# Kernel optimization log

Hardware: AMD Instinct MI355X
Metric: run time of the kernel (lower is better)

Reference implementation:

```python
import jax, jax.numpy as jnp
import numpy as np

B, S, H, E, K = 4, 2048, 1024, 8, 2

def setup_inputs() -> dict:
    key = jax.random.key(0)
    k0, k1, k2, k3 = jax.random.split(key, 4)
    x = jax.random.normal(k0, (B, S, H), dtype=jnp.float32)
    # xavier-uniform-like scales
    router_w = jax.random.normal(k1, (E, H), dtype=jnp.float32) * np.float32(1.0 / np.sqrt(H))
    xav1 = np.float32(np.sqrt(2.0 / (2 * H + H)))
    w1 = jax.random.normal(k2, (E, 2 * H, H), dtype=jnp.float32) * xav1
    w2 = jax.random.normal(k3, (E, H, 2 * H), dtype=jnp.float32) * xav1
    return {"x": x, "router_w": router_w, "w1": w1, "w2": w2}

def reference(x, router_w, w1, w2):
    bsz, seq, hidden = x.shape
    n_experts = w1.shape[0]
    tokens = x.reshape(-1, hidden)                      # [T, H]
    T = tokens.shape[0]
    logits = tokens @ router_w.T                        # [T, E]
    topv, topi = jax.lax.top_k(logits, K)               # [T, K]
    w = jax.nn.softmax(topv, axis=-1).astype(tokens.dtype)
    # Dense gate matrix: gate[t, e] = routing weight of expert e for token t
    # (zero for non-selected experts). Equivalent to the torch pad/dispatch/
    # scatter-add combine: padded slots have weight 0 and contribute nothing.
    gate = jnp.zeros((T, n_experts), tokens.dtype).at[jnp.arange(T)[:, None], topi].add(w)
    out = jnp.zeros_like(tokens)
    for e in range(n_experts):  # small fixed expert count
        h = jax.nn.gelu(tokens @ w1[e].T, approximate=False)  # [T, 2H] (torch F.gelu = erf)
        y = h @ w2[e].T                                       # [T, H]
        out = out + gate[:, e:e + 1] * y
    return out.reshape(bsz, seq, hidden)
```

## Files before the change

### kernel.cpp

```cpp
#include <hip/hip_runtime.h>
#include <stdint.h>
#include <math.h>

#define T_TOK 8192
#define H_DIM 1024
#define H2    2048
#define NE    8

typedef unsigned short u16;
typedef __attribute__((ext_vector_type(8))) short bf16x8;
typedef __attribute__((ext_vector_type(4))) float f32x4;

__device__ __forceinline__ u16 f32_to_bf16(float f) {
  union { float f; unsigned u; } c; c.f = f;
  unsigned u = c.u + 0x7fffu + ((c.u >> 16) & 1u);
  return (u16)(u >> 16);
}
__device__ __forceinline__ float bf2f(u16 v) {
  union { unsigned u; float f; } c; c.u = (unsigned)v << 16; return c.f;
}

__device__ __forceinline__ float fast_gelu(float v) {
  float u = v * v;
  float z2 = v * fmaf(u, 0.1029437f, 2.3022078f);
  float e = __builtin_amdgcn_exp2f(z2);
  float r = __builtin_amdgcn_rcpf(1.0f + e);
  return v - v * r;
}

__device__ __forceinline__ void g2l16(const void* g, void* l) {
  __builtin_amdgcn_global_load_lds(
      (const __attribute__((address_space(1))) unsigned*)g,
      (__attribute__((address_space(3))) unsigned*)l, 16, 0, 0);
}

__global__ __launch_bounds__(256) void prep_kernel(
    const float* __restrict__ x, const float* __restrict__ rw,
    const float* __restrict__ w1, const float* __restrict__ w2,
    u16* __restrict__ xb, u16* __restrict__ w1b, u16* __restrict__ w2b,
    int* __restrict__ tope, float2* __restrict__ gate2) {
  int blk = blockIdx.x;
  if (blk < T_TOK / 4) {
    int wave = threadIdx.x >> 6;
    int lane = threadIdx.x & 63;
    int t = blk * 4 + wave;
    const float4* x4 = (const float4*)(x + (size_t)t * H_DIM);
    const float4* rw4 = (const float4*)rw;
    u16* xbrow = xb + (size_t)t * H_DIM;

    double acc[NE];
#pragma unroll
    for (int e = 0; e < NE; e++) acc[e] = 0.0;
#pragma unroll
    for (int i = 0; i < 4; i++) {
      int c = lane + 64 * i;
      float4 xv = x4[c];
      ushort4 bv = make_ushort4(f32_to_bf16(xv.x), f32_to_bf16(xv.y),
                                f32_to_bf16(xv.z), f32_to_bf16(xv.w));
      *(ushort4*)(xbrow + c * 4) = bv;
#pragma unroll
      for (int e = 0; e < NE; e++) {
        float4 wv = rw4[e * 256 + c];
        acc[e] += (double)xv.x * wv.x + (double)xv.y * wv.y +
                  (double)xv.z * wv.z + (double)xv.w * wv.w;
      }
    }
#pragma unroll
    for (int off = 32; off >= 1; off >>= 1)
#pragma unroll
      for (int e = 0; e < NE; e++) acc[e] += __shfl_xor(acc[e], off, 64);

    if (lane == 0) {
      int e0 = 0; double v0 = acc[0];
#pragma unroll
      for (int e = 1; e < NE; e++) if (acc[e] > v0) { v0 = acc[e]; e0 = e; }
      int e1 = -1; double v1 = -1e300;
#pragma unroll
      for (int e = 0; e < NE; e++) if (e != e0 && acc[e] > v1) { v1 = acc[e]; e1 = e; }
      double ex = exp(v1 - v0);
      tope[t] = e0 | (e1 << 8);
      gate2[t] = make_float2((float)(1.0 / (1.0 + ex)), (float)(ex / (1.0 + ex)));
    }
  } else {
    int cb = blk - T_TOK / 4;
    const float* src; u16* dst;
    if (cb < 1536) { src = w1; dst = w1b; }
    else           { src = w2; dst = w2b; cb -= 1536; }
    const int n4 = NE * H2 * H_DIM / 4;
    const int stride = 1536 * 256;
    const float4* s4 = (const float4*)src;
    for (int i = cb * 256 + threadIdx.x; i < n4; i += stride) {
      float4 v = s4[i];
      *(ushort4*)(dst + (size_t)i * 4) = make_ushort4(
          f32_to_bf16(v.x), f32_to_bf16(v.y), f32_to_bf16(v.z), f32_to_bf16(v.w));
    }
  }
}

__global__ __launch_bounds__(256) void build_kernel(
    const int* __restrict__ tope, int* __restrict__ counts,
    int* __restrict__ tok_list, int2* __restrict__ pos2) {
  __shared__ int cts[4][NE];
  __shared__ int gbase[NE];
  int tid = threadIdx.x, lane = tid & 63, w = tid >> 6;
  int t = blockIdx.x * 256 + tid;
  int pk = tope[t];
  int e0 = pk & 0xff, e1 = (pk >> 8) & 0xff;
  unsigned long long lt = ((unsigned long long)1 << lane) - 1;

  int r0 = 0, r1 = 0;
#pragma unroll
  for (int e = 0; e < NE; e++) {
    unsigned long long b0 = __ballot(e0 == e);
    unsigned long long b1 = __ballot(e1 == e);
    int n0 = __popcll(b0), n1 = __popcll(b1);
    if (e0 == e) r0 = __popcll(b0 & lt);
    if (e1 == e) r1 = n0 + __popcll(b1 & lt);
    if (lane == 0) cts[w][e] = n0 + n1;
  }
  __syncthreads();
  if (tid < NE) {
    int bt = cts[0][tid] + cts[1][tid] + cts[2][tid] + cts[3][tid];
    gbase[tid] = atomicAdd(&counts[tid], bt);
  }
  __syncthreads();
  int off0 = gbase[e0] + r0;
  int off1 = gbase[e1] + r1;
#pragma unroll
  for (int wp = 0; wp < 4; wp++) {
    if (wp < w) { off0 += cts[wp][e0]; off1 += cts[wp][e1]; }
  }
  tok_list[e0 * T_TOK + off0] = t;
  tok_list[e1 * T_TOK + off1] = t;
  pos2[t] = make_int2(off0, off1);
}

__global__ void prefix_kernel(const int* __restrict__ counts, int* __restrict__ hbase) {
  if (threadIdx.x == 0 && blockIdx.x == 0) {
    int b = 0;
    for (int e = 0; e < NE; e++) { hbase[e] = b; b += counts[e]; }
  }
}

__global__ __launch_bounds__(256) void g1_kernel(
    const u16* __restrict__ xb, const u16* __restrict__ w1b,
    u16* __restrict__ h, const int* __restrict__ tok_list,
    const int* __restrict__ counts, const int* __restrict__ hbase) {
  const int NT = H2 / 128;
  int e = blockIdx.x / (64 * NT);
  int rem = blockIdx.x % (64 * NT);
  int mt = rem / NT, nt = rem % NT;
  int cnt = counts[e];
  int m0 = mt * 128;
  if (m0 >= cnt) return;
  int base = hbase[e];

  __shared__ u16 As[128 * 64];
  __shared__ u16 Bs[128 * 64];

  int tid = threadIdx.x;
  int lane = tid & 63, wave = tid >> 6;
  int wr = wave >> 1, wc = wave & 1;
  int quad = lane >> 4, l16 = lane & 15;
  int srow = tid >> 3;
  int cg = (tid & 7) ^ (srow & 7);

  const u16* w1e = w1b + (size_t)e * H2 * H_DIM;
  const u16* ap[4]; const u16* bp[4];
#pragma unroll
  for (int R = 0; R < 4; R++) {
    int r = m0 + R * 32 + srow; if (r > cnt - 1) r = cnt - 1;
    ap[R] = xb + (size_t)tok_list[e * T_TOK + r] * H_DIM + cg * 8;
    bp[R] = w1e + (size_t)(nt * 128 + R * 32 + srow) * H_DIM + cg * 8;
  }

  f32x4 acc[4][4];
#pragma unroll
  for (int i = 0; i < 4; i++)
#pragma unroll
    for (int j = 0; j < 4; j++)
#pragma unroll
      for (int r = 0; r < 4; r++) acc[i][j][r] = 0.f;

  int swz = l16 & 7;
  for (int k0 = 0; k0 < H_DIM; k0 += 64) {
#pragma unroll
    for (int R = 0; R < 4; R++) {
      g2l16(ap[R] + k0, As + R * 2048 + tid * 8);
      g2l16(bp[R] + k0, Bs + R * 2048 + tid * 8);
    }
    __syncthreads();
#pragma unroll
    for (int kk = 0; kk < 2; kk++) {
      bf16x8 af[4], bfr[4];
      int q = kk * 4 + quad;
#pragma unroll
      for (int mi = 0; mi < 4; mi++)
        af[mi] = *(const bf16x8*)(As + (wr * 64 + mi * 16 + l16) * 64 + ((q ^ swz) * 8));
#pragma unroll
      for (int ni = 0; ni < 4; ni++)
        bfr[ni] = *(const bf16x8*)(Bs + (wc * 64 + ni * 16 + l16) * 64 + ((q ^ swz) * 8));
#pragma unroll
      for (int mi = 0; mi < 4; mi++)
#pragma unroll
        for (int ni = 0; ni < 4; ni++)
          acc[mi][ni] = __builtin_amdgcn_mfma_f32_16x16x32_bf16(af[mi], bfr[ni], acc[mi][ni], 0, 0, 0);
    }
    __syncthreads();
  }

#pragma unroll
  for (int mi = 0; mi < 4; mi++) {
    int rbase = wr * 64 + mi * 16 + quad * 4;
#pragma unroll
    for (int r = 0; r < 4; r++) {
      int rr = m0 + rbase + r;
      if (rr < cnt) {
        size_t ho = (size_t)(base + rr) * H2 + nt * 128 + wc * 64 + l16;
#pragma unroll
        for (int ni = 0; ni < 4; ni++)
          h[ho + ni * 16] = f32_to_bf16(fast_gelu(acc[mi][ni][r]));
      }
    }
  }
}

__global__ __launch_bounds__(256) void g2_kernel(
    const u16* __restrict__ h, const u16* __restrict__ w2b,
    u16* __restrict__ y,
    const int* __restrict__ counts, const int* __restrict__ hbase) {
  const int NT = H_DIM / 128;
  int e = blockIdx.x / (64 * NT);
  int rem = blockIdx.x % (64 * NT);
  int mt = rem / NT, nt = rem % NT;
  int cnt = counts[e];
  int m0 = mt * 128;
  if (m0 >= cnt) return;
  int base = hbase[e];

  __shared__ u16 As[128 * 64];
  __shared__ u16 Bs[128 * 64];

  int tid = threadIdx.x;
  int lane = tid & 63, wave = tid >> 6;
  int wr = wave >> 1, wc = wave & 1;
  int quad = lane >> 4, l16 = lane & 15;
  int srow = tid >> 3;
  int cg = (tid & 7) ^ (srow & 7);

  const u16* w2e = w2b + (size_t)e * H_DIM * H2;
  const u16* ap[4]; const u16* bp[4];
#pragma unroll
  for (int R = 0; R < 4; R++) {
    int r = m0 + R * 32 + srow; if (r > cnt - 1) r = cnt - 1;
    ap[R] = h + (size_t)(base + r) * H2 + cg * 8;
    bp[R] = w2e + (size_t)(nt * 128 + R * 32 + srow) * H2 + cg * 8;
  }

  f32x4 acc[4][4];
#pragma unroll
  for (int i = 0; i < 4; i++)
#pragma unroll
    for (int j = 0; j < 4; j++)
#pragma unroll
      for (int r = 0; r < 4; r++) acc[i][j][r] = 0.f;

  int swz = l16 & 7;
  for (int k0 = 0; k0 < H2; k0 += 64) {
#pragma unroll
    for (int R = 0; R < 4; R++) {
      g2l16(ap[R] + k0, As + R * 2048 + tid * 8);
      g2l16(bp[R] + k0, Bs + R * 2048 + tid * 8);
    }
    __syncthreads();
#pragma unroll
    for (int kk = 0; kk < 2; kk++) {
      bf16x8 af[4], bfr[4];
      int q = kk * 4 + quad;
#pragma unroll
      for (int mi = 0; mi < 4; mi++)
        af[mi] = *(const bf16x8*)(As + (wr * 64 + mi * 16 + l16) * 64 + ((q ^ swz) * 8));
#pragma unroll
      for (int ni = 0; ni < 4; ni++)
        bfr[ni] = *(const bf16x8*)(Bs + (wc * 64 + ni * 16 + l16) * 64 + ((q ^ swz) * 8));
#pragma unroll
      for (int mi = 0; mi < 4; mi++)
#pragma unroll
        for (int ni = 0; ni < 4; ni++)
          acc[mi][ni] = __builtin_amdgcn_mfma_f32_16x16x32_bf16(af[mi], bfr[ni], acc[mi][ni], 0, 0, 0);
    }
    __syncthreads();
  }

#pragma unroll
  for (int mi = 0; mi < 4; mi++) {
    int rbase = wr * 64 + mi * 16 + quad * 4;
#pragma unroll
    for (int r = 0; r < 4; r++) {
      int rr = m0 + rbase + r;
      if (rr < cnt) {
        size_t yo = (size_t)(base + rr) * H_DIM + nt * 128 + wc * 64 + l16;
#pragma unroll
        for (int ni = 0; ni < 4; ni++)
          y[yo + ni * 16] = f32_to_bf16(acc[mi][ni][r]);
      }
    }
  }
}

__global__ __launch_bounds__(256) void combine_kernel(
    const u16* __restrict__ y, const int* __restrict__ tope,
    const float2* __restrict__ gate2, const int2* __restrict__ pos2,
    const int* __restrict__ hbase, float* __restrict__ out) {
  int t = blockIdx.x;
  int pk = tope[t];
  int e0 = pk & 0xff, e1 = (pk >> 8) & 0xff;
  float2 g = gate2[t];
  int2 p = pos2[t];
  size_t s0 = (size_t)(hbase[e0] + p.x) * H_DIM + threadIdx.x * 4;
  size_t s1 = (size_t)(hbase[e1] + p.y) * H_DIM + threadIdx.x * 4;
  ushort4 a = *(const ushort4*)(y + s0);
  ushort4 b = *(const ushort4*)(y + s1);
  float4 o;
  o.x = g.x * bf2f(a.x) + g.y * bf2f(b.x);
  o.y = g.x * bf2f(a.y) + g.y * bf2f(b.y);
  o.z = g.x * bf2f(a.z) + g.y * bf2f(b.z);
  o.w = g.x * bf2f(a.w) + g.y * bf2f(b.w);
  *(float4*)(out + (size_t)t * H_DIM + threadIdx.x * 4) = o;
}

extern "C" void kernel_launch(void* const* d_in, const int* in_sizes, int n_in,
                              void* d_out, int out_size, void* d_ws, size_t ws_size,
                              hipStream_t stream) {
  const float* x  = (const float*)d_in[0];
  const float* rw = (const float*)d_in[1];
  const float* w1 = (const float*)d_in[2];
  const float* w2 = (const float*)d_in[3];
  float* out = (float*)d_out;

  char* ws = (char*)d_ws;
  u16* xb       = (u16*)(ws);
  u16* w1b      = (u16*)(ws + 16777216);
  u16* y        = (u16*)(ws + 16777216);
  u16* w2b      = (u16*)(ws + 50331648);
  u16* h        = (u16*)(ws + 83886080);
  int* tok_list = (int*)(ws + 150994944);
  int* tope     = (int*)(ws + 151257088);
  float2* gate2 = (float2*)(ws + 151289856);
  int2* pos2    = (int2*)(ws + 151355392);
  int* counts   = (int*)(ws + 151420928);
  int* hbase    = (int*)(ws + 151420960);

  hipMemsetAsync(counts, 0, 64, stream);
  prep_kernel<<<T_TOK / 4 + 3072, 256, 0, stream>>>(x, rw, w1, w2, xb, w1b, w2b, tope, gate2);
  build_kernel<<<T_TOK / 256, 256, 0, stream>>>(tope, counts, tok_list, pos2);
  prefix_kernel<<<1, 64, 0, stream>>>(counts, hbase);
  g1_kernel<<<NE * 64 * (H2 / 128), 256, 0, stream>>>(xb, w1b, h, tok_list, counts, hbase);
  g2_kernel<<<NE * 64 * (H_DIM / 128), 256, 0, stream>>>(h, w2b, y, counts, hbase);
  combine_kernel<<<T_TOK, 256, 0, stream>>>(y, tope, gate2, pos2, hbase, out);
}
```

Measured before the change: 409.7 us.

## Overlap w2 bf16 conversion with first GEMM and drop prefix kernel

Moves the w2 fp32-to-bf16 conversion from the prep kernel into extra leading blocks of the first expert GEMM kernel, so the conversion overlaps GEMM work instead of lengthening the serial prep phase. The separate prefix-sum kernel is removed; each kernel now computes expert base offsets inline from the counts. The GEMM tile index is reordered so consecutive blocks share an N tile across M tiles, which is meant to improve weight reuse in cache. The risk is that conversion blocks compete with GEMM blocks for bandwidth and compute slots.

Measured after the change: 510.8 us. +24.7%, slower.

```diff
diff --git a/kernel.cpp b/kernel.cpp
--- a/kernel.cpp
+++ b/kernel.cpp
@@ -34,10 +34,17 @@
       (__attribute__((address_space(3))) unsigned*)l, 16, 0, 0);
 }
 
-__global__ __launch_bounds__(256) void prep_kernel(
+__device__ __forceinline__ int prefix_base(const int* counts, int e) {
+  int b = 0;
+#pragma unroll
+  for (int j = 0; j < NE; j++) b += (j < e) ? counts[j] : 0;
+  return b;
+}
+
+__global__ __launch_bounds__(256) void router_kernel(
     const float* __restrict__ x, const float* __restrict__ rw,
-    const float* __restrict__ w1, const float* __restrict__ w2,
-    u16* __restrict__ xb, u16* __restrict__ w1b, u16* __restrict__ w2b,
+    const float* __restrict__ w1,
+    u16* __restrict__ xb, u16* __restrict__ w1b,
     int* __restrict__ tope, float2* __restrict__ gate2) {
   int blk = blockIdx.x;
   if (blk < T_TOK / 4) {
@@ -83,15 +90,12 @@
     }
   } else {
     int cb = blk - T_TOK / 4;
-    const float* src; u16* dst;
-    if (cb < 1536) { src = w1; dst = w1b; }
-    else           { src = w2; dst = w2b; cb -= 1536; }
     const int n4 = NE * H2 * H_DIM / 4;
     const int stride = 1536 * 256;
-    const float4* s4 = (const float4*)src;
+    const float4* s4 = (const float4*)w1;
     for (int i = cb * 256 + threadIdx.x; i < n4; i += stride) {
       float4 v = s4[i];
-      *(ushort4*)(dst + (size_t)i * 4) = make_ushort4(
+      *(ushort4*)(w1b + (size_t)i * 4) = make_ushort4(
           f32_to_bf16(v.x), f32_to_bf16(v.y), f32_to_bf16(v.z), f32_to_bf16(v.w));
     }
   }
@@ -135,25 +139,31 @@
   pos2[t] = make_int2(off0, off1);
 }
 
-__global__ void prefix_kernel(const int* __restrict__ counts, int* __restrict__ hbase) {
-  if (threadIdx.x == 0 && blockIdx.x == 0) {
-    int b = 0;
-    for (int e = 0; e < NE; e++) { hbase[e] = b; b += counts[e]; }
-  }
-}
-
 __global__ __launch_bounds__(256) void g1_kernel(
     const u16* __restrict__ xb, const u16* __restrict__ w1b,
+    const float* __restrict__ w2, u16* __restrict__ w2b,
     u16* __restrict__ h, const int* __restrict__ tok_list,
-    const int* __restrict__ counts, const int* __restrict__ hbase) {
-  const int NT = H2 / 128;
-  int e = blockIdx.x / (64 * NT);
-  int rem = blockIdx.x % (64 * NT);
-  int mt = rem / NT, nt = rem % NT;
+    const int* __restrict__ counts) {
+  if (blockIdx.x < 1536) {
+    int cb = blockIdx.x;
+    const int n4 = NE * H_DIM * H2 / 4;
+    const int stride = 1536 * 256;
+    const float4* s4 = (const float4*)w2;
+    for (int i = cb * 256 + threadIdx.x; i < n4; i += stride) {
+      float4 v = s4[i];
+      *(ushort4*)(w2b + (size_t)i * 4) = make_ushort4(
+          f32_to_bf16(v.x), f32_to_bf16(v.y), f32_to_bf16(v.z), f32_to_bf16(v.w));
+    }
+    return;
+  }
+  int i = blockIdx.x - 1536;
+  int gn = i >> 9;
+  int gm = i & 511;
+  int e = gm >> 6, mt = gm & 63, nt = gn;
   int cnt = counts[e];
   int m0 = mt * 128;
   if (m0 >= cnt) return;
-  int base = hbase[e];
+  int base = prefix_base(counts, e);
 
   __shared__ u16 As[128 * 64];
   __shared__ u16 Bs[128 * 64];
@@ -176,11 +186,11 @@
 
   f32x4 acc[4][4];
 #pragma unroll
-  for (int i = 0; i < 4; i++)
+  for (int i2 = 0; i2 < 4; i2++)
 #pragma unroll
     for (int j = 0; j < 4; j++)
 #pragma unroll
-      for (int r = 0; r < 4; r++) acc[i][j][r] = 0.f;
+      for (int r = 0; r < 4; r++) acc[i2][j][r] = 0.f;
 
   int swz = l16 & 7;
   for (int k0 = 0; k0 < H_DIM; k0 += 64) {
@@ -227,16 +237,15 @@
 
 __global__ __launch_bounds__(256) void g2_kernel(
     const u16* __restrict__ h, const u16* __restrict__ w2b,
-    u16* __restrict__ y,
-    const int* __restrict__ counts, const int* __restrict__ hbase) {
-  const int NT = H_DIM / 128;
-  int e = blockIdx.x / (64 * NT);
-  int rem = blockIdx.x % (64 * NT);
-  int mt = rem / NT, nt = rem % NT;
+    u16* __restrict__ y, const int* __restrict__ counts) {
+  int i = blockIdx.x;
+  int gn = i >> 9;
+  int gm = i & 511;
+  int e = gm >> 6, mt = gm & 63, nt = gn;
   int cnt = counts[e];
   int m0 = mt * 128;
   if (m0 >= cnt) return;
-  int base = hbase[e];
+  int base = prefix_base(counts, e);
 
   __shared__ u16 As[128 * 64];
   __shared__ u16 Bs[128 * 64];
@@ -259,11 +268,11 @@
 
   f32x4 acc[4][4];
 #pragma unroll
-  for (int i = 0; i < 4; i++)
+  for (int i2 = 0; i2 < 4; i2++)
 #pragma unroll
     for (int j = 0; j < 4; j++)
 #pragma unroll
-      for (int r = 0; r < 4; r++) acc[i][j][r] = 0.f;
+      for (int r = 0; r < 4; r++) acc[i2][j][r] = 0.f;
 
   int swz = l16 & 7;
   for (int k0 = 0; k0 < H2; k0 += 64) {
@@ -311,14 +320,16 @@
 __global__ __launch_bounds__(256) void combine_kernel(
     const u16* __restrict__ y, const int* __restrict__ tope,
     const float2* __restrict__ gate2, const int2* __restrict__ pos2,
-    const int* __restrict__ hbase, float* __restrict__ out) {
+    const int* __restrict__ counts, float* __restrict__ out) {
   int t = blockIdx.x;
   int pk = tope[t];
   int e0 = pk & 0xff, e1 = (pk >> 8) & 0xff;
   float2 g = gate2[t];
   int2 p = pos2[t];
-  size_t s0 = (size_t)(hbase[e0] + p.x) * H_DIM + threadIdx.x * 4;
-  size_t s1 = (size_t)(hbase[e1] + p.y) * H_DIM + threadIdx.x * 4;
+  int hb0 = prefix_base(counts, e0);
+  int hb1 = prefix_base(counts, e1);
+  size_t s0 = (size_t)(hb0 + p.x) * H_DIM + threadIdx.x * 4;
+  size_t s1 = (size_t)(hb1 + p.y) * H_DIM + threadIdx.x * 4;
   ushort4 a = *(const ushort4*)(y + s0);
   ushort4 b = *(const ushort4*)(y + s1);
   float4 o;
@@ -349,13 +360,11 @@
   float2* gate2 = (float2*)(ws + 151289856);
   int2* pos2    = (int2*)(ws + 151355392);
   int* counts   = (int*)(ws + 151420928);
-  int* hbase    = (int*)(ws + 151420960);
-
-  hipMemsetAsync(counts, 0, 64, stream);
-  prep_kernel<<<T_TOK / 4 + 3072, 256, 0, stream>>>(x, rw, w1, w2, xb, w1b, w2b, tope, gate2);
+
+  hipMemsetAsync(counts, 0, 32, stream);
+  router_kernel<<<T_TOK / 4 + 1536, 256, 0, stream>>>(x, rw, w1, xb, w1b, tope, gate2);
   build_kernel<<<T_TOK / 256, 256, 0, stream>>>(tope, counts, tok_list, pos2);
-  prefix_kernel<<<1, 64, 0, stream>>>(counts, hbase);
-  g1_kernel<<<NE * 64 * (H2 / 128), 256, 0, stream>>>(xb, w1b, h, tok_list, counts, hbase);
-  g2_kernel<<<NE * 64 * (H_DIM / 128), 256, 0, stream>>>(h, w2b, y, counts, hbase);
-  combine_kernel<<<T_TOK, 256, 0, stream>>>(y, tope, gate2, pos2, hbase, out);
-}
+  g1_kernel<<<1536 + 16 * 512, 256, 0, stream>>>(xb, w1b, w2, w2b, h, tok_list, counts);
+  g2_kernel<<<8 * 512, 256, 0, stream>>>(h, w2b, y, counts);
+  combine_kernel<<<T_TOK, 256, 0, stream>>>(y, tope, gate2, pos2, counts, out);
+}
```
